# Kernel optimization log

Hardware: AMD Instinct MI355X
Metric: run time of the kernel (lower is better)

Reference implementation:

```python
import jax, jax.numpy as jnp
import numpy as np


def setup_inputs() -> dict:
    key = jax.random.key(0)
    k1, k2, k3 = jax.random.split(key, 3)
    B, T1, T2, D, MP = 16, 256, 256, 256, 32
    reps_lt = jax.random.normal(k1, (B, T1, D), dtype=jnp.float32)
    reps_rt = jax.random.normal(k2, (B, T2, D), dtype=jnp.float32)
    # keras 'uniform' initializer ~ U(-0.05, 0.05); stored as [mp, d]
    kernel = jax.random.uniform(k3, (MP, D), dtype=jnp.float32, minval=-0.05, maxval=0.05)
    return {"reps_lt": reps_lt, "reps_rt": reps_rt, "kernel": kernel}


def reference(reps_lt, reps_rt, kernel):
    # reps_lt: [b, t1, d], reps_rt: [b, t2, d], kernel: [mp, d]
    # Original: broadcast lt*kernel -> [b,t1,1,mp,d], rt -> [b,1,t2,1,d],
    # cosine_norm=False => tanh(sum over d), then max over t1.
    lt_m = reps_lt[:, :, None, :] * kernel[None, None, :, :]      # [b, t1, mp, d]
    scores = jnp.einsum('bimd,bjd->bijm', lt_m, reps_rt)           # [b, t1, t2, mp]
    match = jnp.tanh(scores)
    return jnp.max(match, axis=1)                                  # [b, t2, mp]
```

## Files before the change

### kernel.cpp

```cpp
#include <hip/hip_runtime.h>
#include <hip/hip_bf16.h>
#include <math.h>

#define Bn   16
#define T1n  256
#define T2n  256
#define Dn   256
#define MPn  32

typedef __attribute__((ext_vector_type(8))) short short8;
typedef __attribute__((ext_vector_type(4))) float f32x4;

__device__ inline short f2b(float f) {
  __hip_bfloat16 h = __float2bfloat16(f);
  return __builtin_bit_cast(short, h);
}
__device__ inline float b2f(short s) {
  unsigned int u = ((unsigned int)(unsigned short)s) << 16;
  return __builtin_bit_cast(float, u);
}

__device__ inline int swz_chunk(int row, int d8) {
  return row * 32 + (d8 ^ (row & 7));
}

__global__ __launch_bounds__(256, 2)
void mp_match_kernel(const float* __restrict__ lt,
                     const float* __restrict__ rt,
                     const float* __restrict__ kern,
                     float* __restrict__ out) {
  __shared__ short lds_rt[64 * 256];
  __shared__ short lds_lt[64 * 256];

  const int bid  = blockIdx.x;
  const int xcd  = bid & 7;
  const int q    = bid >> 3;
  const int widx = q & 31;
  const int b    = ((q >> 5) << 3) | xcd;
  const int jblk = widx & 3;
  const int mg   = widx >> 2;
  const int j0   = jblk * 64;

  const int tid  = threadIdx.x;
  const int lane = tid & 63;
  const int w    = tid >> 6;
  const int m    = mg * 4 + w;

  const int bl = lane & 15;
  const int hl = lane >> 4;

  {
    const float* rbase = rt + ((size_t)b * T2n + j0) * Dn;
    #pragma unroll
    for (int rep = 0; rep < 8; ++rep) {
      int chunk = rep * 256 + tid;
      int row = chunk >> 5, c = chunk & 31;
      const f32x4* s = reinterpret_cast<const f32x4*>(rbase + row * Dn + c * 8);
      f32x4 f0 = s[0], f1 = s[1];
      short8 v;
      v[0] = f2b(f0.x); v[1] = f2b(f0.y); v[2] = f2b(f0.z); v[3] = f2b(f0.w);
      v[4] = f2b(f1.x); v[5] = f2b(f1.y); v[6] = f2b(f1.z); v[7] = f2b(f1.w);
      *reinterpret_cast<short8*>(&lds_rt[swz_chunk(row, c) * 8]) = v;
    }
  }
  __syncthreads();

  short8 bsc[4][8];
  {
    const float* kbase = kern + (size_t)m * Dn;
    #pragma unroll
    for (int kk = 0; kk < 8; ++kk) {
      int d8 = kk * 4 + hl;
      const f32x4* kp = reinterpret_cast<const f32x4*>(kbase + d8 * 8);
      f32x4 k0 = kp[0], k1 = kp[1];
      #pragma unroll
      for (int sub = 0; sub < 4; ++sub) {
        int brow = sub * 16 + bl;
        short8 r = *reinterpret_cast<const short8*>(&lds_rt[swz_chunk(brow, d8) * 8]);
        short8 v;
        v[0] = f2b(b2f(r[0]) * k0.x); v[1] = f2b(b2f(r[1]) * k0.y);
        v[2] = f2b(b2f(r[2]) * k0.z); v[3] = f2b(b2f(r[3]) * k0.w);
        v[4] = f2b(b2f(r[4]) * k1.x); v[5] = f2b(b2f(r[5]) * k1.y);
        v[6] = f2b(b2f(r[6]) * k1.z); v[7] = f2b(b2f(r[7]) * k1.w);
        bsc[sub][kk] = v;
      }
    }
  }

  float jmax0 = -1e30f, jmax1 = -1e30f, jmax2 = -1e30f, jmax3 = -1e30f;

  for (int ic = 0; ic < 4; ++ic) {
    if (ic) __syncthreads();
    const float* lbase = lt + ((size_t)b * T1n + ic * 64) * Dn;
    #pragma unroll
    for (int rep = 0; rep < 8; ++rep) {
      int chunk = rep * 256 + tid;
      int row = chunk >> 5, c = chunk & 31;
      const f32x4* s = reinterpret_cast<const f32x4*>(lbase + row * Dn + c * 8);
      f32x4 f0 = s[0], f1 = s[1];
      short8 v;
      v[0] = f2b(f0.x); v[1] = f2b(f0.y); v[2] = f2b(f0.z); v[3] = f2b(f0.w);
      v[4] = f2b(f1.x); v[5] = f2b(f1.y); v[6] = f2b(f1.z); v[7] = f2b(f1.w);
      *reinterpret_cast<short8*>(&lds_lt[swz_chunk(row, c) * 8]) = v;
    }
    __syncthreads();

    #pragma unroll
    for (int it = 0; it < 4; ++it) {
      f32x4 acc0 = {0.f,0.f,0.f,0.f}, acc1 = {0.f,0.f,0.f,0.f};
      f32x4 acc2 = {0.f,0.f,0.f,0.f}, acc3 = {0.f,0.f,0.f,0.f};
      int arow = it * 16 + bl;
      #pragma unroll
      for (int kk = 0; kk < 8; ++kk) {
        int d8 = kk * 4 + hl;
        short8 a = *reinterpret_cast<const short8*>(&lds_lt[swz_chunk(arow, d8) * 8]);
        acc0 = __builtin_amdgcn_mfma_f32_16x16x32_bf16(a, bsc[0][kk], acc0, 0, 0, 0);
        acc1 = __builtin_amdgcn_mfma_f32_16x16x32_bf16(a, bsc[1][kk], acc1, 0, 0, 0);
        acc2 = __builtin_amdgcn_mfma_f32_16x16x32_bf16(a, bsc[2][kk], acc2, 0, 0, 0);
        acc3 = __builtin_amdgcn_mfma_f32_16x16x32_bf16(a, bsc[3][kk], acc3, 0, 0, 0);
      }
      jmax0 = fmaxf(jmax0, fmaxf(fmaxf(acc0.x, acc0.y), fmaxf(acc0.z, acc0.w)));
      jmax1 = fmaxf(jmax1, fmaxf(fmaxf(acc1.x, acc1.y), fmaxf(acc1.z, acc1.w)));
      jmax2 = fmaxf(jmax2, fmaxf(fmaxf(acc2.x, acc2.y), fmaxf(acc2.z, acc2.w)));
      jmax3 = fmaxf(jmax3, fmaxf(fmaxf(acc3.x, acc3.y), fmaxf(acc3.z, acc3.w)));
    }
  }

  jmax0 = fmaxf(jmax0, __shfl_xor(jmax0, 16));
  jmax0 = fmaxf(jmax0, __shfl_xor(jmax0, 32));
  jmax1 = fmaxf(jmax1, __shfl_xor(jmax1, 16));
  jmax1 = fmaxf(jmax1, __shfl_xor(jmax1, 32));
  jmax2 = fmaxf(jmax2, __shfl_xor(jmax2, 16));
  jmax2 = fmaxf(jmax2, __shfl_xor(jmax2, 32));
  jmax3 = fmaxf(jmax3, __shfl_xor(jmax3, 16));
  jmax3 = fmaxf(jmax3, __shfl_xor(jmax3, 32));

  if (lane < 16) {
    out[((size_t)b * T2n + (j0 +  0 + lane)) * MPn + m] = tanhf(jmax0);
    out[((size_t)b * T2n + (j0 + 16 + lane)) * MPn + m] = tanhf(jmax1);
    out[((size_t)b * T2n + (j0 + 32 + lane)) * MPn + m] = tanhf(jmax2);
    out[((size_t)b * T2n + (j0 + 48 + lane)) * MPn + m] = tanhf(jmax3);
  }
}

extern "C" void kernel_launch(void* const* d_in, const int* in_sizes, int n_in,
                              void* d_out, int out_size, void* d_ws, size_t ws_size,
                              hipStream_t stream) {
  const float* lt   = (const float*)d_in[0];
  const float* rt   = (const float*)d_in[1];
  const float* kern = (const float*)d_in[2];
  float* out = (float*)d_out;

  dim3 grid(Bn * 4 * (MPn / 4));
  dim3 block(256);
  mp_match_kernel<<<grid, block, 0, stream>>>(lt, rt, kern, out);
}
```

Baseline: 24.44 us.

## Pre-convert inputs to bf16 and double-buffer LDS loads via global_load_lds

Adds a separate kernel that converts lt and rt to bf16 in the workspace once, so the match kernel no longer redoes the fp32-to-bf16 conversion for every block that reads them. The match kernel now uses 512-thread blocks with 8 waves covering 8 match dimensions each, and loads pre-swizzled bf16 tiles straight into LDS with global_load_lds. The lt tiles are double-buffered so the next chunk's load overlaps MFMA work. The output store now uses all lanes. The cost is an extra kernel launch, an extra pass over workspace memory, twice the LDS per block, and fewer blocks in the grid.

```diff
diff --git a/kernel.cpp b/kernel.cpp
--- a/kernel.cpp
+++ b/kernel.cpp
@@ -10,6 +10,13 @@
 
 typedef __attribute__((ext_vector_type(8))) short short8;
 typedef __attribute__((ext_vector_type(4))) float f32x4;
+
+typedef const __attribute__((address_space(1))) void* gp_t;
+typedef __attribute__((address_space(3))) void* lp_t;
+
+__device__ __forceinline__ void gl_lds16(const void* g, void* l) {
+  __builtin_amdgcn_global_load_lds((gp_t)g, (lp_t)l, 16, 0, 0);
+}
 
 __device__ inline short f2b(float f) {
   __hip_bfloat16 h = __float2bfloat16(f);
@@ -24,19 +31,36 @@
   return row * 32 + (d8 ^ (row & 7));
 }
 
-__global__ __launch_bounds__(256, 2)
-void mp_match_kernel(const float* __restrict__ lt,
-                     const float* __restrict__ rt,
+__global__ __launch_bounds__(256, 8)
+void cvt_bf16_kernel(const float* __restrict__ lt, const float* __restrict__ rt,
+                     short* __restrict__ olt, short* __restrict__ ort) {
+  int blk = blockIdx.x;
+  const float* src;
+  short* dst;
+  int t;
+  if (blk < 512) { src = lt; dst = olt; t = blk * 256 + threadIdx.x; }
+  else           { src = rt; dst = ort; t = (blk - 512) * 256 + threadIdx.x; }
+  const f32x4* s = reinterpret_cast<const f32x4*>(src + (size_t)t * 8);
+  f32x4 f0 = s[0], f1 = s[1];
+  short8 v;
+  v[0] = f2b(f0.x); v[1] = f2b(f0.y); v[2] = f2b(f0.z); v[3] = f2b(f0.w);
+  v[4] = f2b(f1.x); v[5] = f2b(f1.y); v[6] = f2b(f1.z); v[7] = f2b(f1.w);
+  *reinterpret_cast<short8*>(dst + (size_t)t * 8) = v;
+}
+
+__global__ __launch_bounds__(512, 2)
+void mp_match_kernel(const short* __restrict__ ltb,
+                     const short* __restrict__ rtb,
                      const float* __restrict__ kern,
                      float* __restrict__ out) {
   __shared__ short lds_rt[64 * 256];
-  __shared__ short lds_lt[64 * 256];
+  __shared__ short lds_lt[2][64 * 256];
 
   const int bid  = blockIdx.x;
   const int xcd  = bid & 7;
   const int q    = bid >> 3;
-  const int widx = q & 31;
-  const int b    = ((q >> 5) << 3) | xcd;
+  const int widx = q & 15;
+  const int b    = ((q >> 4) << 3) | xcd;
   const int jblk = widx & 3;
   const int mg   = widx >> 2;
   const int j0   = jblk * 64;
@@ -44,26 +68,31 @@
   const int tid  = threadIdx.x;
   const int lane = tid & 63;
   const int w    = tid >> 6;
-  const int m    = mg * 4 + w;
+  const int m    = mg * 8 + w;
+  const int bl   = lane & 15;
+  const int hl   = lane >> 4;
 
-  const int bl = lane & 15;
-  const int hl = lane >> 4;
+  int soff[4];
+  #pragma unroll
+  for (int it = 0; it < 4; ++it) {
+    int cidx = it * 512 + tid;
+    int row = cidx >> 5, slot = cidx & 31;
+    int c = slot ^ (row & 7);
+    soff[it] = row * 256 + c * 8;
+  }
+  const int cb0 = (tid & ~63) * 8;
 
-  {
-    const float* rbase = rt + ((size_t)b * T2n + j0) * Dn;
-    #pragma unroll
-    for (int rep = 0; rep < 8; ++rep) {
-      int chunk = rep * 256 + tid;
-      int row = chunk >> 5, c = chunk & 31;
-      const f32x4* s = reinterpret_cast<const f32x4*>(rbase + row * Dn + c * 8);
-      f32x4 f0 = s[0], f1 = s[1];
-      short8 v;
-      v[0] = f2b(f0.x); v[1] = f2b(f0.y); v[2] = f2b(f0.z); v[3] = f2b(f0.w);
-      v[4] = f2b(f1.x); v[5] = f2b(f1.y); v[6] = f2b(f1.z); v[7] = f2b(f1.w);
-      *reinterpret_cast<short8*>(&lds_rt[swz_chunk(row, c) * 8]) = v;
-    }
-  }
+  const short* rbase = rtb + ((size_t)b * T2n + j0) * Dn;
+  #pragma unroll
+  for (int it = 0; it < 4; ++it)
+    gl_lds16(rbase + soff[it], &lds_rt[it * 512 * 8 + cb0]);
+  asm volatile("s_waitcnt vmcnt(0)" ::: "memory");
   __syncthreads();
+
+  const short* lbase = ltb + (size_t)b * T1n * Dn;
+  #pragma unroll
+  for (int it = 0; it < 4; ++it)
+    gl_lds16(lbase + soff[it], &lds_lt[0][it * 512 * 8 + cb0]);
 
   short8 bsc[4][8];
   {
@@ -89,31 +118,27 @@
 
   float jmax0 = -1e30f, jmax1 = -1e30f, jmax2 = -1e30f, jmax3 = -1e30f;
 
+  asm volatile("s_waitcnt vmcnt(0)" ::: "memory");
+  __syncthreads();
+
   for (int ic = 0; ic < 4; ++ic) {
-    if (ic) __syncthreads();
-    const float* lbase = lt + ((size_t)b * T1n + ic * 64) * Dn;
+    const int cur = ic & 1;
+    if (ic < 3) {
+      #pragma unroll
+      for (int it = 0; it < 4; ++it)
+        gl_lds16(lbase + (ic + 1) * 64 * 256 + soff[it],
+                 &lds_lt[cur ^ 1][it * 512 * 8 + cb0]);
+    }
+    const short* lcur = lds_lt[cur];
     #pragma unroll
-    for (int rep = 0; rep < 8; ++rep) {
-      int chunk = rep * 256 + tid;
-      int row = chunk >> 5, c = chunk & 31;
-      const f32x4* s = reinterpret_cast<const f32x4*>(lbase + row * Dn + c * 8);
-      f32x4 f0 = s[0], f1 = s[1];
-      short8 v;
-      v[0] = f2b(f0.x); v[1] = f2b(f0.y); v[2] = f2b(f0.z); v[3] = f2b(f0.w);
-      v[4] = f2b(f1.x); v[5] = f2b(f1.y); v[6] = f2b(f1.z); v[7] = f2b(f1.w);
-      *reinterpret_cast<short8*>(&lds_lt[swz_chunk(row, c) * 8]) = v;
-    }
-    __syncthreads();
-
-    #pragma unroll
-    for (int it = 0; it < 4; ++it) {
+    for (int it2 = 0; it2 < 4; ++it2) {
       f32x4 acc0 = {0.f,0.f,0.f,0.f}, acc1 = {0.f,0.f,0.f,0.f};
       f32x4 acc2 = {0.f,0.f,0.f,0.f}, acc3 = {0.f,0.f,0.f,0.f};
-      int arow = it * 16 + bl;
+      int arow = it2 * 16 + bl;
       #pragma unroll
       for (int kk = 0; kk < 8; ++kk) {
         int d8 = kk * 4 + hl;
-        short8 a = *reinterpret_cast<const short8*>(&lds_lt[swz_chunk(arow, d8) * 8]);
+        short8 a = *reinterpret_cast<const short8*>(&lcur[swz_chunk(arow, d8) * 8]);
         acc0 = __builtin_amdgcn_mfma_f32_16x16x32_bf16(a, bsc[0][kk], acc0, 0, 0, 0);
         acc1 = __builtin_amdgcn_mfma_f32_16x16x32_bf16(a, bsc[1][kk], acc1, 0, 0, 0);
         acc2 = __builtin_amdgcn_mfma_f32_16x16x32_bf16(a, bsc[2][kk], acc2, 0, 0, 0);
@@ -123,6 +148,10 @@
       jmax1 = fmaxf(jmax1, fmaxf(fmaxf(acc1.x, acc1.y), fmaxf(acc1.z, acc1.w)));
       jmax2 = fmaxf(jmax2, fmaxf(fmaxf(acc2.x, acc2.y), fmaxf(acc2.z, acc2.w)));
       jmax3 = fmaxf(jmax3, fmaxf(fmaxf(acc3.x, acc3.y), fmaxf(acc3.z, acc3.w)));
+    }
+    if (ic < 3) {
+      asm volatile("s_waitcnt vmcnt(0)" ::: "memory");
+      __syncthreads();
     }
   }
 
@@ -134,13 +163,9 @@
   jmax2 = fmaxf(jmax2, __shfl_xor(jmax2, 32));
   jmax3 = fmaxf(jmax3, __shfl_xor(jmax3, 16));
   jmax3 = fmaxf(jmax3, __shfl_xor(jmax3, 32));
-
-  if (lane < 16) {
-    out[((size_t)b * T2n + (j0 +  0 + lane)) * MPn + m] = tanhf(jmax0);
-    out[((size_t)b * T2n + (j0 + 16 + lane)) * MPn + m] = tanhf(jmax1);
-    out[((size_t)b * T2n + (j0 + 32 + lane)) * MPn + m] = tanhf(jmax2);
-    out[((size_t)b * T2n + (j0 + 48 + lane)) * MPn + m] = tanhf(jmax3);
-  }
+  float v = (hl == 0) ? jmax0 : (hl == 1) ? jmax1 : (hl == 2) ? jmax2 : jmax3;
+  int j = j0 + hl * 16 + bl;
+  out[((size_t)b * T2n + j) * MPn + m] = tanhf(v);
 }
 
 extern "C" void kernel_launch(void* const* d_in, const int* in_sizes, int n_in,
@@ -151,7 +176,9 @@
   const float* kern = (const float*)d_in[2];
   float* out = (float*)d_out;
 
-  dim3 grid(Bn * 4 * (MPn / 4));
-  dim3 block(256);
-  mp_match_kernel<<<grid, block, 0, stream>>>(lt, rt, kern, out);
+  short* ltb = (short*)d_ws;
+  short* rtb = ltb + (size_t)Bn * T1n * Dn;
+
+  cvt_bf16_kernel<<<1024, 256, 0, stream>>>(lt, rt, ltb, rtb);
+  mp_match_kernel<<<256, 512, 0, stream>>>(ltb, rtb, kern, out);
 }
```

Measured after the change: 26.70 us. +9.3%, slower.
